# Kernel optimization log

Hardware: AMD Instinct MI355X
Metric: run time of the kernel (lower is better)

Reference implementation:

```python
import jax, jax.numpy as jnp
import numpy as np

B, N, F, H, F_ = 4, 2048, 64, 4, 64


def setup_inputs() -> dict:
    key = jax.random.key(0)
    kx, ka, kw, ks, kn = jax.random.split(key, 5)
    X = jax.random.normal(kx, (B, N, F), dtype=jnp.float32)
    A = (jax.random.uniform(ka, (B, N, N)) < 0.05).astype(jnp.float32)
    A = jnp.maximum(A, jnp.eye(N, dtype=jnp.float32)[None])
    W = jax.random.normal(kw, (H, F, F_), dtype=jnp.float32) * 0.1
    a_self = jax.random.normal(ks, (H, F_), dtype=jnp.float32) * 0.1
    a_neigh = jax.random.normal(kn, (H, F_), dtype=jnp.float32) * 0.1
    return {"X": X, "A": A, "W": W, "a_self": a_self, "a_neigh": a_neigh}


def reference(X, A, W, a_self, a_neigh):
    # linear transform per head: [B,H,N,F_]
    lin = jnp.einsum('bnf,hfo->bhno', X, W)
    # additive attention scores
    s_self = jnp.einsum('bhno,ho->bhn', lin, a_self)[:, :, :, None]   # [B,H,N,1]
    s_neigh = jnp.einsum('bhno,ho->bhn', lin, a_neigh)[:, :, None, :]  # [B,H,1,N]
    dense = s_self + s_neigh                                           # [B,H,N,N]
    dense = jnp.where(dense >= 0, dense, 0.2 * dense)                  # LeakyReLU(0.2)
    BIG = jnp.float32(1e10)
    mask = jnp.exp(A * -BIG) * -BIG                                    # 0 where edge, -1e10 where no edge
    logits = dense + mask[:, None, :, :]
    attn = jax.nn.softmax(logits, axis=-1)
    # dropout is identity at inference (attn_dropout=0.0)
    feats = jnp.einsum('bhnm,bhmo->bhno', attn, lin)                   # [B,H,N,F_]
    feats = jax.nn.relu(feats)                                         # activation before concat
    b, h, n, f_ = feats.shape
    out = feats.transpose(0, 2, 1, 3).reshape(b, n, h * f_)            # concat heads
    return out
```

## Files before the change

### kernel.cpp

```cpp
#include <hip/hip_runtime.h>
#include <hip/hip_bf16.h>

#define BB 4
#define NN 2048
#define FF 64
#define HH 4
#define FO 64
#define CAP 256


__global__ __launch_bounds__(256) void BatchGraphAttention_84378927497895_kernel(
    const float* __restrict__ W, const float* __restrict__ a_self,
    const float* __restrict__ a_neigh, float* __restrict__ w_self,
    float* __restrict__ w_neigh) {
  int t = threadIdx.x;
  int h = t >> 6;
  const float* Wp = W + t * FO;
  const float* as = a_self + h * FO;
  const float* an = a_neigh + h * FO;
  float acc_s = 0.f, acc_n = 0.f;
#pragma unroll
  for (int o = 0; o < FO; ++o) {
    float w = Wp[o];
    acc_s += w * as[o];
    acc_n += w * an[o];
  }
  w_self[t] = acc_s;
  w_neigh[t] = acc_n;
}

__global__ __launch_bounds__(256) void BatchGraphAttention_84378927497895_kernel2(
    const float* __restrict__ X, const float* __restrict__ w_self,
    const float* __restrict__ w_neigh, float* __restrict__ s_self,
    float* __restrict__ s_neigh) {
  int bn = blockIdx.x;
  int t = threadIdx.x, h = t >> 6, f = t & 63;
  float x = X[(size_t)bn * FF + f];
  float vs = x * w_self[h * FF + f];
  float vn = x * w_neigh[h * FF + f];
#pragma unroll
  for (int off = 32; off > 0; off >>= 1) {
    vs += __shfl_down(vs, off, 64);
    vn += __shfl_down(vn, off, 64);
  }
  if (f == 0) {
    int b = bn >> 11, n = bn & (NN - 1);
    int bh = b * HH + h;
    s_self[bh * NN + n] = vs;
    s_neigh[bh * NN + n] = vn;
  }
}

__global__ __launch_bounds__(256) void BatchGraphAttention_84378927497895_kernel3(
    const float* __restrict__ A, const float* __restrict__ X,
    const float* __restrict__ W, const float* __restrict__ s_self,
    const float* __restrict__ s_neigh, float* __restrict__ out) {
  int bn = blockIdx.x;
  int b = bn >> 11;
  int n = bn & (NN - 1);
  __shared__ unsigned short idx[CAP];
  __shared__ float plt[CAP][4];
  __shared__ float red[4][HH][FF];
  __shared__ float ys[HH][FF];
  __shared__ float sinv[HH];
  __shared__ int cnt_s;
  int t = threadIdx.x;
  int lane = t & 63, wv = t >> 6;
  if (t == 0) cnt_s = 0;
  __syncthreads();

  {
    const float4* Ar4 = (const float4*)(A + (size_t)bn * NN);
#pragma unroll
    for (int it = 0; it < 2; ++it) {
      int q = t + it * 256;
      float4 v = Ar4[q];
      unsigned base = (unsigned)q * 4u;
      if (v.x != 0.f) { int p = atomicAdd(&cnt_s, 1); if (p < CAP) idx[p] = (unsigned short)(base + 0); }
      if (v.y != 0.f) { int p = atomicAdd(&cnt_s, 1); if (p < CAP) idx[p] = (unsigned short)(base + 1); }
      if (v.z != 0.f) { int p = atomicAdd(&cnt_s, 1); if (p < CAP) idx[p] = (unsigned short)(base + 2); }
      if (v.w != 0.f) { int p = atomicAdd(&cnt_s, 1); if (p < CAP) idx[p] = (unsigned short)(base + 3); }
    }
  }
  __syncthreads();
  int cnt = cnt_s;
  if (cnt > CAP) cnt = CAP;

  {
    int h = wv;
    int bh = b * HH + h;
    float ss = s_self[bh * NN + n];
    const float* snp = s_neigh + (size_t)bh * NN;

    float lmax = -1e30f;
    for (int j = lane; j < cnt; j += 64) {
      float lg = ss + snp[idx[j]];
      lg = (lg >= 0.f) ? lg : 0.2f * lg;
      plt[j][h] = lg;
      lmax = fmaxf(lmax, lg);
    }
#pragma unroll
    for (int off = 32; off > 0; off >>= 1)
      lmax = fmaxf(lmax, __shfl_xor(lmax, off, 64));

    float lsum = 0.f;
    for (int j = lane; j < cnt; j += 64) {
      float e = __expf(plt[j][h] - lmax);
      plt[j][h] = e;
      lsum += e;
    }
#pragma unroll
    for (int off = 32; off > 0; off >>= 1) lsum += __shfl_xor(lsum, off, 64);
    if (lane == 0) sinv[h] = 1.f / lsum;
  }
  __syncthreads();

  {
    const float* xp = X + (size_t)b * NN * FF + lane;
    float y0 = 0.f, y1 = 0.f, y2 = 0.f, y3 = 0.f;
    int j = wv;
    for (; j + 12 < cnt; j += 16) {
      int m0 = idx[j], m1 = idx[j + 4], m2 = idx[j + 8], m3 = idx[j + 12];
      float4 p0 = *(const float4*)plt[j];
      float4 p1 = *(const float4*)plt[j + 4];
      float4 p2 = *(const float4*)plt[j + 8];
      float4 p3 = *(const float4*)plt[j + 12];
      float x0 = xp[m0 * FF];
      float x1 = xp[m1 * FF];
      float x2 = xp[m2 * FF];
      float x3 = xp[m3 * FF];
      y0 += p0.x * x0; y1 += p0.y * x0; y2 += p0.z * x0; y3 += p0.w * x0;
      y0 += p1.x * x1; y1 += p1.y * x1; y2 += p1.z * x1; y3 += p1.w * x1;
      y0 += p2.x * x2; y1 += p2.y * x2; y2 += p2.z * x2; y3 += p2.w * x2;
      y0 += p3.x * x3; y1 += p3.y * x3; y2 += p3.z * x3; y3 += p3.w * x3;
    }
    for (; j < cnt; j += 4) {
      float4 p = *(const float4*)plt[j];
      float x = xp[idx[j] * FF];
      y0 += p.x * x; y1 += p.y * x; y2 += p.z * x; y3 += p.w * x;
    }
    red[wv][0][lane] = y0;
    red[wv][1][lane] = y1;
    red[wv][2][lane] = y2;
    red[wv][3][lane] = y3;
  }
  __syncthreads();

  {
    int h = wv, f = lane;
    float s = red[0][h][f] + red[1][h][f] + red[2][h][f] + red[3][h][f];
    ys[h][f] = s * sinv[h];
  }
  __syncthreads();
  {
    const float* Wp = W + wv * FF * FO + lane;
    float acc = 0.f;
#pragma unroll
    for (int f = 0; f < FF; ++f) acc += ys[wv][f] * Wp[f * FO];
    acc = (acc > 0.f) ? acc : 0.f;
    out[(size_t)bn * (HH * FO) + t] = acc;
  }
}

extern "C" void kernel_launch(void* const* d_in, const int* in_sizes, int n_in,
                              void* d_out, int out_size, void* d_ws,
                              size_t ws_size, hipStream_t stream) {
  const float* X = (const float*)d_in[0];
  const float* A = (const float*)d_in[1];
  const float* W = (const float*)d_in[2];
  const float* a_self = (const float*)d_in[3];
  const float* a_neigh = (const float*)d_in[4];
  float* out = (float*)d_out;

  float* w_self = (float*)d_ws;
  float* w_neigh = w_self + HH * FF;
  float* s_self = w_neigh + HH * FF;
  float* s_neigh = s_self + (size_t)BB * HH * NN;

  BatchGraphAttention_84378927497895_kernel<<<1, 256, 0, stream>>>(
      W, a_self, a_neigh, w_self, w_neigh);
  BatchGraphAttention_84378927497895_kernel2<<<BB * NN, 256, 0, stream>>>(
      X, w_self, w_neigh, s_self, s_neigh);
  BatchGraphAttention_84378927497895_kernel3<<<BB * NN, 256, 0, stream>>>(
      A, X, W, s_self, s_neigh, out);
}
```

Measured before the change: 148.3 us.

## Split output projection into separate kernel with W cached in registers

The per-row multiply by W is moved out of the attention-aggregation kernel. The attention kernel now writes the normalized aggregated X features into the output buffer, and a new kernel applies W in place, 16 rows per block, with each thread holding its W column in registers. This avoids every one of the 8192 blocks re-reading W from cache and drops one barrier plus shared staging. In exchange it adds a kernel launch and a global write and read of the intermediate. The in-place update depends on each head's 64 threads running as a single wave, so all reads of a row finish before any write to it.

```diff
diff --git a/kernel.cpp b/kernel.cpp
--- a/kernel.cpp
+++ b/kernel.cpp
@@ -53,16 +53,14 @@
 
 __global__ __launch_bounds__(256) void BatchGraphAttention_84378927497895_kernel3(
     const float* __restrict__ A, const float* __restrict__ X,
-    const float* __restrict__ W, const float* __restrict__ s_self,
-    const float* __restrict__ s_neigh, float* __restrict__ out) {
+    const float* __restrict__ s_self, const float* __restrict__ s_neigh,
+    float* __restrict__ outScratch) {
   int bn = blockIdx.x;
   int b = bn >> 11;
   int n = bn & (NN - 1);
   __shared__ unsigned short idx[CAP];
   __shared__ float plt[CAP][4];
   __shared__ float red[4][HH][FF];
-  __shared__ float ys[HH][FF];
-  __shared__ float sinv[HH];
   __shared__ int cnt_s;
   int t = threadIdx.x;
   int lane = t & 63, wv = t >> 6;
@@ -86,6 +84,7 @@
   int cnt = cnt_s;
   if (cnt > CAP) cnt = CAP;
 
+  float inv;
   {
     int h = wv;
     int bh = b * HH + h;
@@ -111,7 +110,7 @@
     }
 #pragma unroll
     for (int off = 32; off > 0; off >>= 1) lsum += __shfl_xor(lsum, off, 64);
-    if (lane == 0) sinv[h] = 1.f / lsum;
+    inv = 1.f / lsum;
   }
   __syncthreads();
 
@@ -149,16 +148,35 @@
   {
     int h = wv, f = lane;
     float s = red[0][h][f] + red[1][h][f] + red[2][h][f] + red[3][h][f];
-    ys[h][f] = s * sinv[h];
-  }
-  __syncthreads();
-  {
-    const float* Wp = W + wv * FF * FO + lane;
+    outScratch[(size_t)bn * (HH * FO) + t] = s * inv;
+  }
+}
+
+#define K4_ROWS 16
+__global__ __launch_bounds__(256) void BatchGraphAttention_84378927497895_kernel4(
+    const float* __restrict__ W, float* out) {
+  int t = threadIdx.x;
+  int h = t >> 6, o = t & 63;
+  float w[FF];
+  {
+    const float* Wp = W + h * FF * FO + o;
+#pragma unroll
+    for (int f = 0; f < FF; ++f) w[f] = Wp[f * FO];
+  }
+  size_t base = (size_t)blockIdx.x * K4_ROWS;
+  for (int r = 0; r < K4_ROWS; ++r) {
+    const float4* yg = (const float4*)(out + (base + r) * (HH * FO) + h * FO);
     float acc = 0.f;
 #pragma unroll
-    for (int f = 0; f < FF; ++f) acc += ys[wv][f] * Wp[f * FO];
+    for (int fq = 0; fq < FF / 4; ++fq) {
+      float4 y4 = yg[fq];
+      acc += w[4 * fq + 0] * y4.x;
+      acc += w[4 * fq + 1] * y4.y;
+      acc += w[4 * fq + 2] * y4.z;
+      acc += w[4 * fq + 3] * y4.w;
+    }
     acc = (acc > 0.f) ? acc : 0.f;
-    out[(size_t)bn * (HH * FO) + t] = acc;
+    out[(base + r) * (HH * FO) + t] = acc;
   }
 }
 
@@ -182,5 +200,7 @@
   BatchGraphAttention_84378927497895_kernel2<<<BB * NN, 256, 0, stream>>>(
       X, w_self, w_neigh, s_self, s_neigh);
   BatchGraphAttention_84378927497895_kernel3<<<BB * NN, 256, 0, stream>>>(
-      A, X, W, s_self, s_neigh, out);
-}
+      A, X, s_self, s_neigh, out);
+  BatchGraphAttention_84378927497895_kernel4<<<(BB * NN) / K4_ROWS, 256, 0, stream>>>(
+      W, out);
+}
```

Measured after the change: 153.0 us. +3.2%, slower.
